# Optimization experiments

Measured on AMD Instinct MI355X. Metric: run time of the kernel, lower is better.

## Reference

```python
import jax, jax.numpy as jnp
import numpy as np

EPS = 1e-5
C = 256
K = 3
K2 = K * K


def conv2d(x, w, b=None, groups=1):
    out = jax.lax.conv_general_dilated(
        x, w, (1, 1), 'VALID',
        dimension_numbers=('NCHW', 'OIHW', 'NCHW'),
        feature_group_count=groups)
    if b is not None:
        out = out + b[None, :, None, None]
    return out


def _bilinear_one(img, py, px):
    # img: [C,H,W]; py,px: [K2,ho,wo] float sampling coords (zero outside)
    _, H, W = img.shape
    y0 = jnp.floor(py)
    x0 = jnp.floor(px)
    dy = py - y0
    dx = px - x0
    y0i = y0.astype(jnp.int32)
    x0i = x0.astype(jnp.int32)

    def gather(yi, xi):
        valid = ((yi >= 0) & (yi < H) & (xi >= 0) & (xi < W)).astype(img.dtype)
        yc = jnp.clip(yi, 0, H - 1)
        xc = jnp.clip(xi, 0, W - 1)
        return img[:, yc, xc] * valid[None]  # [C,K2,ho,wo]

    w00 = (1 - dy) * (1 - dx)
    w01 = (1 - dy) * dx
    w10 = dy * (1 - dx)
    w11 = dy * dx
    return (gather(y0i, x0i) * w00[None] + gather(y0i, x0i + 1) * w01[None]
            + gather(y0i + 1, x0i) * w10[None] + gather(y0i + 1, x0i + 1) * w11[None])


def deform_conv(x, off_w, off_b, w, b):
    # ModulatedDeformConvPack: 3x3, stride=1, pad=0, dil=1, deformable_groups=1
    B, Cin, H, W = x.shape
    ho, wo = H - 2, W - 2
    om = conv2d(x, off_w, off_b)  # [B, 3*K2, ho, wo]
    o1, o2, m = om[:, :K2], om[:, K2:2 * K2], om[:, 2 * K2:]
    offset = jnp.concatenate([o1, o2], axis=1)  # [B, 2*K2, ho, wo]
    off_y = offset[:, 0::2]  # kernel reads y at channel 2k
    off_x = offset[:, 1::2]  # and x at channel 2k+1
    mask = jax.nn.sigmoid(m)  # [B,K2,ho,wo]
    ky, kx = jnp.meshgrid(jnp.arange(K), jnp.arange(K), indexing='ij')
    base_y = (ky.reshape(K2, 1, 1) + jnp.arange(ho).reshape(1, ho, 1)).astype(x.dtype)
    base_x = (kx.reshape(K2, 1, 1) + jnp.arange(wo).reshape(1, 1, wo)).astype(x.dtype)
    py = base_y[None] + off_y
    px = base_x[None] + off_x
    samples = jax.vmap(_bilinear_one)(x, py, px)  # [B,C,K2,ho,wo]
    samples = samples * mask[:, None]
    out = jnp.einsum('bckhw,ock->bohw', samples, w.reshape(w.shape[0], Cin, K2))
    return out + b[None, :, None, None]


def bn(x, g, b_, m, v):
    scale = g / jnp.sqrt(v + EPS)
    return (x - m[None, :, None, None]) * scale[None, :, None, None] + b_[None, :, None, None]


def xcorr(inst, exam):
    # batch-as-groups depthwise cross-correlation
    B = exam.shape[0]
    w = exam.reshape(B * C, 1, 18, 18)
    x = inst.reshape(1, B * C, 30, 30)
    out = jax.lax.conv_general_dilated(
        x, w, (1, 1), 'VALID',
        dimension_numbers=('NCHW', 'OIHW', 'NCHW'),
        feature_group_count=B * C)
    return out.reshape(B, C, 13, 13)


def _forward(examplar, instance, off_w, off_b, dcn_w, dcn_b,
             bn1_g, bn1_b, bn1_m, bn1_v,
             fus_w, fus_b, bn2_g, bn2_b, bn2_m, bn2_v,
             cls_w, cls_b, box_w, box_b):
    def head(x, i):  # deform conv + BN (eval)
        y = deform_conv(x, off_w[i], off_b[i], dcn_w[i], dcn_b[i])
        return bn(y, bn1_g[i], bn1_b[i], bn1_m[i], bn1_v[i])

    exam_cls = head(examplar, 0)
    inst_cls = head(instance, 1)
    exam_reg = head(examplar, 2)
    inst_reg = head(instance, 3)

    xc_cls = xcorr(inst_cls, exam_cls)
    xc_reg = xcorr(inst_reg, exam_reg)

    def fuse(x, i):  # 1x1 conv + BN + ReLU
        y = jnp.einsum('bchw,oc->bohw', x, fus_w[i]) + fus_b[i][None, :, None, None]
        return jax.nn.relu(bn(y, bn2_g[i], bn2_b[i], bn2_m[i], bn2_v[i]))

    f_cls = fuse(xc_cls, 0)
    f_reg = fuse(xc_reg, 1)

    cls_pred = jnp.einsum('bchw,oc->bohw', f_cls, cls_w) + cls_b[None, :, None, None]
    box_pred = jnp.einsum('bchw,oc->bohw', f_reg, box_w) + box_b[None, :, None, None]
    return cls_pred, box_pred


def setup_inputs() -> dict:
    key = jax.random.key(0)
    ks = jax.random.split(key, 24)
    B = 16
    d = {
        'examplar': jax.random.normal(ks[0], (B, C, 20, 20), jnp.float32),
        'instance': jax.random.normal(ks[1], (B, C, 32, 32), jnp.float32),
        # 4 deform heads: 0=exam_cls, 1=inst_cls, 2=exam_reg, 3=inst_reg
        'off_w': jax.random.normal(ks[2], (4, 3 * K2, C, K, K), jnp.float32) * 0.01,
        'off_b': jax.random.normal(ks[3], (4, 3 * K2), jnp.float32) * 0.01,
        'dcn_w': jax.random.normal(ks[4], (4, C, C, K, K), jnp.float32) * 0.05,
        'dcn_b': jax.random.normal(ks[5], (4, C), jnp.float32) * 0.05,
        'bn1_g': jax.random.uniform(ks[6], (4, C), jnp.float32) + 0.5,
        'bn1_b': jax.random.normal(ks[7], (4, C), jnp.float32) * 0.1,
        'bn1_m': jax.random.normal(ks[8], (4, C), jnp.float32) * 0.1,
        'bn1_v': jax.random.uniform(ks[9], (4, C), jnp.float32) + 0.5,
        # 2 fusion modules: 0=cls, 1=reg
        'fus_w': jax.random.normal(ks[10], (2, C, C), jnp.float32) * 0.05,
        'fus_b': jax.random.normal(ks[11], (2, C), jnp.float32) * 0.05,
        'bn2_g': jax.random.uniform(ks[12], (2, C), jnp.float32) + 0.5,
        'bn2_b': jax.random.normal(ks[13], (2, C), jnp.float32) * 0.1,
        'bn2_m': jax.random.normal(ks[14], (2, C), jnp.float32) * 0.1,
        'bn2_v': jax.random.uniform(ks[15], (2, C), jnp.float32) + 0.5,
        'cls_w': jax.random.normal(ks[16], (4, C), jnp.float32) * 0.05,
        'cls_b': jax.random.normal(ks[17], (4,), jnp.float32) * 0.05,
        'box_w': jax.random.normal(ks[18], (16, C), jnp.float32) * 0.05,
        'box_b': jax.random.normal(ks[19], (16,), jnp.float32) * 0.05,
    }
    return d


def reference(examplar, instance, off_w, off_b, dcn_w, dcn_b,
              bn1_g, bn1_b, bn1_m, bn1_v,
              fus_w, fus_b, bn2_g, bn2_b, bn2_m, bn2_v,
              cls_w, cls_b, box_w, box_b):
    return _forward(examplar, instance, off_w, off_b, dcn_w, dcn_b,
                    bn1_g, bn1_b, bn1_m, bn1_v,
                    fus_w, fus_b, bn2_g, bn2_b, bn2_m, bn2_v,
                    cls_w, cls_b, box_w, box_b)
```

## Files before the change

kernel.cpp:

```cpp
#include <hip/hip_runtime.h>
#include <math.h>

#define EPSBN 1e-5f

typedef _Float16 f16x8 __attribute__((ext_vector_type(8)));
typedef _Float16 f16x2 __attribute__((ext_vector_type(2)));
typedef float    f32x4 __attribute__((ext_vector_type(4)));

__device__ __forceinline__ f16x8 splat8(float v) {
  _Float16 h = (_Float16)v;
  return (f16x8){h, h, h, h, h, h, h, h};
}

__device__ __forceinline__ void tile_decode(int idx, int& h, int& tl) {
  if (idx < 6)       { h = 0; tl = idx; }
  else if (idx < 21) { h = 1; tl = idx - 6; }
  else if (idx < 27) { h = 2; tl = idx - 21; }
  else               { h = 3; tl = idx - 27; }
}

static constexpr size_t XF_EX = 0;
static constexpr size_t XF_IN = 819200;
static constexpr size_t WPK   = 2916352;
static constexpr size_t OWPK  = 4096000;
static constexpr size_t FWT   = 4243456;
static constexpr size_t OM0   = 4374528;
static constexpr size_t OM1   = 4514496;
static constexpr size_t OM2   = 4903296;
static constexpr size_t OM3   = 5043264;
static constexpr size_t HOUT0 = 5432064;
static constexpr size_t HOUT1 = 6759168;
static constexpr size_t HOUT2 = 10445568;
static constexpr size_t HOUT3 = 11772672;
static constexpr size_t XCB   = 15459072;

__global__ __launch_bounds__(256) void k_transpose(const float* __restrict__ in,
                                                   _Float16* __restrict__ out,
                                                   int H, int W) {
  int y = blockIdx.x, b = blockIdx.y;
  __shared__ float tile[32][257];
  int t = threadIdx.x;
  int x = t & 31, cb = t >> 5;
  for (int c0 = 0; c0 < 256; c0 += 8) {
    int c = c0 + cb;
    if (x < W) tile[x][c] = in[(((size_t)b * 256 + c) * H + y) * W + x];
  }
  __syncthreads();
  for (int x2 = 0; x2 < W; ++x2)
    out[((((size_t)b * H + y) * W + x2) << 8) + t] = (_Float16)tile[x2][t];
}

__global__ __launch_bounds__(256) void k_wpack(const float* __restrict__ w,
                                               _Float16* __restrict__ wp) {
  int idx = blockIdx.x * 256 + threadIdx.x;
  if (idx >= 4 * 9 * 8 * 16 * 64 * 8) return;
  int e  = idx & 7;
  int l  = (idx >> 3) & 63;
  int ot = (idx >> 9) & 15;
  int cs = (idx >> 13) & 7;
  int ht = idx >> 16;
  int tap = ht % 9, h = ht / 9;
  int o = ot * 16 + (l & 15);
  int c = cs * 32 + 8 * (l >> 4) + e;
  wp[idx] = (_Float16)w[((size_t)((h * 256 + o) * 256 + c)) * 9 + tap];
}

__global__ __launch_bounds__(256) void k_owpack(const float* __restrict__ w,
                                                _Float16* __restrict__ wp) {
  int idx = blockIdx.x * 256 + threadIdx.x;
  if (idx >= 4 * 9 * 8 * 2 * 64 * 8) return;
  int e  = idx & 7;
  int l  = (idx >> 3) & 63;
  int ot = (idx >> 9) & 1;
  int cs = (idx >> 10) & 7;
  int ht = idx >> 13;
  int tap = ht % 9, h = ht / 9;
  int o = ot * 16 + (l & 15);
  int c = cs * 32 + 8 * (l >> 4) + e;
  wp[idx] = (o < 27) ? (_Float16)w[((size_t)((h * 27 + o) * 256 + c)) * 9 + tap]
                     : (_Float16)0.f;
}

__global__ __launch_bounds__(256) void k_fwt(const float* __restrict__ w,
                                             float* __restrict__ wt) {
  int idx = blockIdx.x * 256 + threadIdx.x;
  int o = idx & 255, c = (idx >> 8) & 255, i = idx >> 16;
  wt[idx] = w[(i << 16) + (o << 8) + c];
}

__global__ __launch_bounds__(512) void k_offmfma(const _Float16* __restrict__ xh_ex,
                                                 const _Float16* __restrict__ xh_in,
                                                 const _Float16* __restrict__ owpk,
                                                 const float* __restrict__ off_b,
                                                 float* __restrict__ ws) {
  int h, tl;
  tile_decode(blockIdx.x, h, tl);
  const int b = blockIdx.y;
  const int HH[4] = {20, 32, 20, 32};
  const size_t OMO[4] = {OM0, OM1, OM2, OM3};
  const int H = HH[h], W = H, ho = H - 2, wo = W - 2, P = ho * wo;
  const int p0 = tl << 6;
  const _Float16* xh = ((h & 1) ? xh_in : xh_ex) + (((size_t)b * H * W) << 8);

  __shared__ __align__(16) _Float16 S[64 * 256];
  __shared__ int rowoff[64];

  const int t = threadIdx.x, lane = t & 63, wave = t >> 6;
  if (t < 64) {
    int p = min(p0 + t, P - 1);
    int i = p / wo, j = p - i * wo;
    rowoff[t] = (i * W + j) << 8;
  }
  const int ot = wave & 1, nn = wave >> 1;
  f32x4 acc = {0.f, 0.f, 0.f, 0.f};
  __syncthreads();

  const int o8 = t & 31;
  const int plb = t >> 5;
  for (int tap = 0; tap < 9; ++tap) {
    const int ky = tap / 3, kx = tap - ky * 3;
    const int koff = (ky * W + kx) << 8;
    #pragma unroll
    for (int it = 0; it < 4; ++it) {
      int pl = it * 16 + plb;
      f16x8 v = *(const f16x8*)(xh + rowoff[pl] + koff + o8 * 8);
      *(f16x8*)((char*)S + pl * 512 + ((o8 * 16) ^ ((pl & 7) << 4))) = v;
    }
    __syncthreads();
    #pragma unroll
    for (int cs = 0; cs < 8; ++cs) {
      int ksg = tap * 8 + cs;
      const _Float16* ab = owpk + ((size_t)((h * 72 + ksg) * 2 + ot)) * 512 + lane * 8;
      f16x8 a = *(const f16x8*)(ab);
      int prow = nn * 16 + (lane & 15);
      f16x8 bf = *(const f16x8*)((char*)S + prow * 512 +
                                 ((cs * 64 + ((lane >> 4) << 4)) ^ ((prow & 7) << 4)));
      acc = __builtin_amdgcn_mfma_f32_16x16x32_f16(a, bf, acc, 0, 0, 0);
    }
    __syncthreads();
  }
  float* om = ws + OMO[h] + (size_t)b * 27 * P;
  int p = p0 + nn * 16 + (lane & 15);
  if (p < P) {
    #pragma unroll
    for (int r = 0; r < 4; ++r) {
      int o = ot * 16 + 4 * (lane >> 4) + r;
      if (o < 27) om[o * P + p] = acc[r] + off_b[h * 27 + o];
    }
  }
}

__global__ __launch_bounds__(512) void k_dgemm(const _Float16* __restrict__ xh_ex,
                                               const _Float16* __restrict__ xh_in,
                                               const _Float16* __restrict__ wpk,
                                               float* __restrict__ ws,
                                               const float* __restrict__ dcn_b,
                                               const float* __restrict__ g1,
                                               const float* __restrict__ b1,
                                               const float* __restrict__ m1,
                                               const float* __restrict__ v1) {
  int h, tl;
  tile_decode(blockIdx.x, h, tl);
  const int HH4[4] = {20, 32, 20, 32};
  const size_t OMO[4] = {OM0, OM1, OM2, OM3};
  const size_t HOO[4] = {HOUT0, HOUT1, HOUT2, HOUT3};
  const int H = HH4[h], W = H, ho = H - 2, wo = W - 2, P = ho * wo;
  const int b = blockIdx.y;
  const int p0 = tl << 6;
  const _Float16* xh = (h & 1) ? xh_in : xh_ex;
  const float* om = ws + OMO[h] + (size_t)b * 27 * P;
  float* outp = ws + HOO[h] + (size_t)b * 256 * P;

  __shared__ float4 swt4[576];
  __shared__ int4   sad4[576];
  __shared__ __align__(16) _Float16 S[64 * 256];

  const int t = threadIdx.x, lane = t & 63, wave = t >> 6;

  for (int e = t; e < 576; e += 512) {
    int pl = e / 9, k = e - pl * 9;
    float w4[4] = {0.f, 0.f, 0.f, 0.f};
    int a4[4] = {0, 0, 0, 0};
    int p = p0 + pl;
    if (p < P) {
      int i = p / wo, j = p - i * wo;
      float oy = om[(2 * k) * P + p];
      float ox = om[(2 * k + 1) * P + p];
      float mm = om[(18 + k) * P + p];
      float msk = 1.f / (1.f + __expf(-mm));
      int ky = k / 3, kx = k - ky * 3;
      float py = (float)(ky + i) + oy;
      float px = (float)(kx + j) + ox;
      float fy = floorf(py), fx = floorf(px);
      int y0 = (int)fy, x0 = (int)fx;
      float dy = py - fy, dx = px - fx;
      #pragma unroll
      for (int q = 0; q < 4; ++q) {
        int yy = y0 + (q >> 1), xx = x0 + (q & 1);
        bool vld = (yy >= 0) && (yy < H) && (xx >= 0) && (xx < W);
        int yc = min(max(yy, 0), H - 1), xc = min(max(xx, 0), W - 1);
        float wq = ((q >> 1) ? dy : 1.f - dy) * ((q & 1) ? dx : 1.f - dx);
        w4[q] = vld ? wq * msk : 0.f;
        a4[q] = ((b * H + yc) * W + xc) << 8;
      }
    }
    swt4[e] = make_float4(w4[0], w4[1], w4[2], w4[3]);
    sad4[e] = make_int4(a4[0], a4[1], a4[2], a4[3]);
  }

  f32x4 acc[2][4];
  #pragma unroll
  for (int a = 0; a < 2; ++a)
    #pragma unroll
    for (int n = 0; n < 4; ++n) acc[a][n] = (f32x4){0.f, 0.f, 0.f, 0.f};

  __syncthreads();

  const int o8 = t & 31;
  const int plb = t >> 5;
  for (int tap = 0; tap < 9; ++tap) {
    #pragma unroll
    for (int it = 0; it < 4; ++it) {
      int pl = it * 16 + plb;
      float4 w4 = swt4[pl * 9 + tap];
      int4   a4 = sad4[pl * 9 + tap];
      const _Float16* xb = xh + o8 * 8;
      f16x8 x0 = *(const f16x8*)(xb + a4.x);
      f16x8 x1 = *(const f16x8*)(xb + a4.y);
      f16x8 x2 = *(const f16x8*)(xb + a4.z);
      f16x8 x3 = *(const f16x8*)(xb + a4.w);
      f16x8 s = x0 * splat8(w4.x) + x1 * splat8(w4.y) + x2 * splat8(w4.z) + x3 * splat8(w4.w);
      *(f16x8*)((char*)S + pl * 512 + ((o8 * 16) ^ ((pl & 7) << 4))) = s;
    }
    __syncthreads();
    #pragma unroll
    for (int cs = 0; cs < 8; ++cs) {
      int ksg = tap * 8 + cs;
      const _Float16* ab = wpk + ((size_t)(h * 72 + ksg) * 16 + wave * 2) * 512 + lane * 8;
      f16x8 A0 = *(const f16x8*)(ab);
      f16x8 A1 = *(const f16x8*)(ab + 512);
      f16x8 B[4];
      #pragma unroll
      for (int n = 0; n < 4; ++n) {
        int prow = n * 16 + (lane & 15);
        B[n] = *(const f16x8*)((char*)S + prow * 512 +
                               ((cs * 64 + ((lane >> 4) << 4)) ^ ((prow & 7) << 4)));
      }
      #pragma unroll
      for (int n = 0; n < 4; ++n) {
        acc[0][n] = __builtin_amdgcn_mfma_f32_16x16x32_f16(A0, B[n], acc[0][n], 0, 0, 0);
        acc[1][n] = __builtin_amdgcn_mfma_f32_16x16x32_f16(A1, B[n], acc[1][n], 0, 0, 0);
      }
    }
    __syncthreads();
  }

  #pragma unroll
  for (int a = 0; a < 2; ++a) {
    int obase = (wave * 2 + a) * 16 + 4 * (lane >> 4);
    #pragma unroll
    for (int r = 0; r < 4; ++r) {
      int o = obase + r;
      float al = g1[h * 256 + o] * rsqrtf(v1[h * 256 + o] + EPSBN);
      float be = (dcn_b[h * 256 + o] - m1[h * 256 + o]) * al + b1[h * 256 + o];
      #pragma unroll
      for (int n = 0; n < 4; ++n) {
        int p = p0 + n * 16 + (lane & 15);
        if (p < P) outp[(size_t)o * P + p] = fmaf(acc[a][n][r], al, be);
      }
    }
  }
}

__global__ __launch_bounds__(256) void k_xcorr3(float* __restrict__ ws) {
  const int br = blockIdx.y;
  const int bc0 = blockIdx.x << 4;
  const float* exg = ws + (br ? HOUT2 : HOUT0) + (size_t)bc0 * 324;
  const float* ing = ws + (br ? HOUT3 : HOUT1) + (size_t)bc0 * 900;
  __shared__ __align__(16) _Float16 exl[16 * 324];
  __shared__ __align__(16) _Float16 inl[16 * 960];
  const int t = threadIdx.x;
  for (int idx = t; idx < 16 * 324; idx += 256)
    exl[idx] = (_Float16)exg[idx];
  for (int idx = t; idx < 16 * 960; idx += 256) {
    int c = idx & 31;
    int rr = idx >> 5;
    inl[idx] = (c < 30) ? (_Float16)ing[rr * 30 + c] : (_Float16)0.f;
  }
  __syncthreads();
  const int lane = t & 63, wave = t >> 6;
  const int sub = lane / 13;
  const int i = lane - sub * 13;
  const bool active = sub < 4;
  const int bcl = wave * 4 + (active ? sub : 0);
  float acc[13];
  #pragma unroll
  for (int j = 0; j < 13; ++j) acc[j] = 0.f;
  const _Float16* inb = inl + bcl * 960;
  const _Float16* exb = exl + bcl * 324;
  for (int u = 0; u < 18; ++u) {
    float a[30];
    const _Float16* rp = inb + (i + u) * 32;
    #pragma unroll
    for (int x = 0; x < 15; ++x) {
      f16x2 pr = *(const f16x2*)(rp + 2 * x);
      a[2 * x] = (float)pr[0]; a[2 * x + 1] = (float)pr[1];
    }
    float e[18];
    const _Float16* ep = exb + u * 18;
    #pragma unroll
    for (int x = 0; x < 9; ++x) {
      f16x2 pr = *(const f16x2*)(ep + 2 * x);
      e[2 * x] = (float)pr[0]; e[2 * x + 1] = (float)pr[1];
    }
    #pragma unroll
    for (int v = 0; v < 18; ++v)
      #pragma unroll
      for (int j = 0; j < 13; ++j)
        acc[j] = fmaf(a[v + j], e[v], acc[j]);
  }
  if (active) {
    float* o = ws + XCB + ((size_t)(br * 4096 + bc0 + bcl)) * 169 + i * 13;
    #pragma unroll
    for (int j = 0; j < 13; ++j) o[j] = acc[j];
  }
}

__global__ __launch_bounds__(256) void k_fuse2(float* __restrict__ ws,
                                               const float* __restrict__ fus_b,
                                               const float* __restrict__ g2,
                                               const float* __restrict__ b2,
                                               const float* __restrict__ m2,
                                               const float* __restrict__ v2,
                                               const float* __restrict__ cls_w,
                                               const float* __restrict__ cls_b,
                                               const float* __restrict__ box_w,
                                               const float* __restrict__ box_b,
                                               float* __restrict__ out) {
  const int ij0 = blockIdx.x * 13;
  const int b = blockIdx.y;
  const int br = blockIdx.z;
  const int n_out = br ? 16 : 4;
  const float* ow = br ? box_w : cls_w;
  const float* ob = br ? box_b : cls_b;
  float* outp = out + (br ? (size_t)10816 : 0);

  __shared__ float xv[256 * 13];
  __shared__ float fv[13 * 257];
  const int t = threadIdx.x;
  const float* src = ws + XCB + ((size_t)br * 4096 + b * 256) * 169;
  for (int idx = t; idx < 256 * 13; idx += 256) {
    int c = idx / 13, j = idx - c * 13;
    xv[idx] = src[(size_t)c * 169 + ij0 + j];
  }
  __syncthreads();

  const float* fwt = ws + FWT + ((size_t)br << 16) + t;
  float acc[13];
  #pragma unroll
  for (int j = 0; j < 13; ++j) acc[j] = 0.f;
  for (int c = 0; c < 256; ++c) {
    float wv = fwt[c << 8];
    #pragma unroll
    for (int j = 0; j < 13; ++j)
      acc[j] = fmaf(wv, xv[c * 13 + j], acc[j]);
  }
  float s2 = g2[br * 256 + t] * rsqrtf(v2[br * 256 + t] + EPSBN);
  float fb = fus_b[br * 256 + t], mm = m2[br * 256 + t], bb = b2[br * 256 + t];
  #pragma unroll
  for (int j = 0; j < 13; ++j)
    fv[j * 257 + t] = fmaxf((acc[j] + fb - mm) * s2 + bb, 0.f);
  __syncthreads();

  const int g = t >> 4, l16 = t & 15;
  for (int wi = g; wi < 13 * n_out; wi += 16) {
    int j = wi / n_out, po = wi - j * n_out;
    float part = 0.f;
    #pragma unroll
    for (int q = 0; q < 16; ++q)
      part = fmaf(ow[(po << 8) + l16 + (q << 4)], fv[j * 257 + l16 + (q << 4)], part);
    #pragma unroll
    for (int off = 8; off; off >>= 1) part += __shfl_xor(part, off);
    if (l16 == 0)
      outp[((size_t)b * n_out + po) * 169 + ij0 + j] = part + ob[po];
  }
}

extern "C" void kernel_launch(void* const* d_in, const int* in_sizes, int n_in,
                              void* d_out, int out_size, void* d_ws, size_t ws_size,
                              hipStream_t stream) {
  const float* ex    = (const float*)d_in[0];
  const float* inst  = (const float*)d_in[1];
  const float* off_w = (const float*)d_in[2];
  const float* off_b = (const float*)d_in[3];
  const float* dcn_w = (const float*)d_in[4];
  const float* dcn_b = (const float*)d_in[5];
  const float* bn1_g = (const float*)d_in[6];
  const float* bn1_b = (const float*)d_in[7];
  const float* bn1_m = (const float*)d_in[8];
  const float* bn1_v = (const float*)d_in[9];
  const float* fus_w = (const float*)d_in[10];
  const float* fus_b = (const float*)d_in[11];
  const float* bn2_g = (const float*)d_in[12];
  const float* bn2_b = (const float*)d_in[13];
  const float* bn2_m = (const float*)d_in[14];
  const float* bn2_v = (const float*)d_in[15];
  const float* cls_w = (const float*)d_in[16];
  const float* cls_b = (const float*)d_in[17];
  const float* box_w = (const float*)d_in[18];
  const float* box_b = (const float*)d_in[19];
  float* out = (float*)d_out;
  float* ws  = (float*)d_ws;

  _Float16* xh_ex = (_Float16*)(ws + XF_EX);
  _Float16* xh_in = (_Float16*)(ws + XF_IN);
  _Float16* wpk   = (_Float16*)(ws + WPK);
  _Float16* owpk  = (_Float16*)(ws + OWPK);

  k_transpose<<<dim3(20, 16), 256, 0, stream>>>(ex,   xh_ex, 20, 20);
  k_transpose<<<dim3(32, 16), 256, 0, stream>>>(inst, xh_in, 32, 32);
  k_wpack <<<9216, 256, 0, stream>>>(dcn_w, wpk);
  k_owpack<<<1152, 256, 0, stream>>>(off_w, owpk);
  k_fwt   <<<512, 256, 0, stream>>>(fus_w, ws + FWT);
  k_offmfma<<<dim3(42, 16), 512, 0, stream>>>(xh_ex, xh_in, owpk, off_b, ws);
  k_dgemm<<<dim3(42, 16), 512, 0, stream>>>(xh_ex, xh_in, wpk, ws,
                                            dcn_b, bn1_g, bn1_b, bn1_m, bn1_v);
  k_xcorr3<<<dim3(256, 2), 256, 0, stream>>>(ws);
  k_fuse2<<<dim3(13, 16, 2), 256, 0, stream>>>(ws, fus_b, bn2_g, bn2_b, bn2_m, bn2_v,
                                               cls_w, cls_b, box_w, box_b, out);
}
```

Baseline: 330.1 us.

## Fuse offset conv into deformable GEMM kernel and prefetch next-tap gathers

Merges the offset/mask convolution kernel into the deformable GEMM kernel, so offsets for each 64-pixel tile stay in shared memory instead of going through a global workspace. It also software-pipelines both tap loops by loading the next tap's inputs into registers while the MFMAs for the current tap run. Launch bounds now request 4 blocks per CU, and the grid becomes 1D with batch folded in. The costs are more registers (16 f16x8 prefetch buffers), more shared memory per block, and the offset conv being recomputed per tile exactly as before, with one fewer launch.

```diff
diff --git a/kernel.cpp b/kernel.cpp
--- a/kernel.cpp
+++ b/kernel.cpp
@@ -10,13 +10,6 @@
 __device__ __forceinline__ f16x8 splat8(float v) {
   _Float16 h = (_Float16)v;
   return (f16x8){h, h, h, h, h, h, h, h};
-}
-
-__device__ __forceinline__ void tile_decode(int idx, int& h, int& tl) {
-  if (idx < 6)       { h = 0; tl = idx; }
-  else if (idx < 21) { h = 1; tl = idx - 6; }
-  else if (idx < 27) { h = 2; tl = idx - 21; }
-  else               { h = 3; tl = idx - 27; }
 }
 
 static constexpr size_t XF_EX = 0;
@@ -24,10 +17,6 @@
 static constexpr size_t WPK   = 2916352;
 static constexpr size_t OWPK  = 4096000;
 static constexpr size_t FWT   = 4243456;
-static constexpr size_t OM0   = 4374528;
-static constexpr size_t OM1   = 4514496;
-static constexpr size_t OM2   = 4903296;
-static constexpr size_t OM3   = 5043264;
 static constexpr size_t HOUT0 = 5432064;
 static constexpr size_t HOUT1 = 6759168;
 static constexpr size_t HOUT2 = 10445568;
@@ -88,94 +77,91 @@
   wt[idx] = w[(i << 16) + (o << 8) + c];
 }
 
-__global__ __launch_bounds__(512) void k_offmfma(const _Float16* __restrict__ xh_ex,
+__global__ __launch_bounds__(512, 4) void k_head(const _Float16* __restrict__ xh_ex,
                                                  const _Float16* __restrict__ xh_in,
                                                  const _Float16* __restrict__ owpk,
+                                                 const _Float16* __restrict__ wpk,
                                                  const float* __restrict__ off_b,
-                                                 float* __restrict__ ws) {
-  int h, tl;
-  tile_decode(blockIdx.x, h, tl);
-  const int b = blockIdx.y;
-  const int HH[4] = {20, 32, 20, 32};
-  const size_t OMO[4] = {OM0, OM1, OM2, OM3};
-  const int H = HH[h], W = H, ho = H - 2, wo = W - 2, P = ho * wo;
+                                                 float* __restrict__ ws,
+                                                 const float* __restrict__ dcn_b,
+                                                 const float* __restrict__ g1,
+                                                 const float* __restrict__ b1,
+                                                 const float* __restrict__ m1,
+                                                 const float* __restrict__ v1) {
+  int idx = blockIdx.x;
+  int h, b, tl;
+  if (idx < 96)       { h = 0; b = idx / 6;              tl = idx - 6 * b; }
+  else if (idx < 336) { h = 1; int r = idx - 96;  b = r / 15; tl = r - 15 * b; }
+  else if (idx < 432) { h = 2; int r = idx - 336; b = r / 6;  tl = r - 6 * b; }
+  else                { h = 3; int r = idx - 432; b = r / 15; tl = r - 15 * b; }
+  const int HH4[4] = {20, 32, 20, 32};
+  const size_t HOO[4] = {HOUT0, HOUT1, HOUT2, HOUT3};
+  const int H = HH4[h], W = H, ho = H - 2, wo = W - 2, P = ho * wo;
   const int p0 = tl << 6;
-  const _Float16* xh = ((h & 1) ? xh_in : xh_ex) + (((size_t)b * H * W) << 8);
+  const _Float16* xh  = (h & 1) ? xh_in : xh_ex;
+  const _Float16* xhb = xh + (((size_t)b * H * W) << 8);
+  float* outp = ws + HOO[h] + (size_t)b * 256 * P;
 
   __shared__ __align__(16) _Float16 S[64 * 256];
-  __shared__ int rowoff[64];
+  __shared__ float4 swt4[576];
+  __shared__ int4   sad4[576];
+  __shared__ float  om_l[27][65];
+  __shared__ int    rowoff[64];
 
   const int t = threadIdx.x, lane = t & 63, wave = t >> 6;
+  const int o8 = t & 31, plb = t >> 5;
+  const int ot = wave & 1, nn = wave >> 1;
+
   if (t < 64) {
     int p = min(p0 + t, P - 1);
     int i = p / wo, j = p - i * wo;
     rowoff[t] = (i * W + j) << 8;
   }
-  const int ot = wave & 1, nn = wave >> 1;
-  f32x4 acc = {0.f, 0.f, 0.f, 0.f};
-  __syncthreads();
-
-  const int o8 = t & 31;
-  const int plb = t >> 5;
+  __syncthreads();
+
+  f32x4 accO = {0.f, 0.f, 0.f, 0.f};
+  f16x8 gr[4];
+  #pragma unroll
+  for (int it = 0; it < 4; ++it) {
+    int pl = it * 16 + plb;
+    gr[it] = *(const f16x8*)(xhb + rowoff[pl] + o8 * 8);
+  }
   for (int tap = 0; tap < 9; ++tap) {
-    const int ky = tap / 3, kx = tap - ky * 3;
-    const int koff = (ky * W + kx) << 8;
     #pragma unroll
     for (int it = 0; it < 4; ++it) {
       int pl = it * 16 + plb;
-      f16x8 v = *(const f16x8*)(xh + rowoff[pl] + koff + o8 * 8);
-      *(f16x8*)((char*)S + pl * 512 + ((o8 * 16) ^ ((pl & 7) << 4))) = v;
+      *(f16x8*)((char*)S + pl * 512 + ((o8 * 16) ^ ((pl & 7) << 4))) = gr[it];
     }
     __syncthreads();
+    if (tap < 8) {
+      int ky = (tap + 1) / 3, kx = (tap + 1) - ky * 3;
+      int koff = (ky * W + kx) << 8;
+      #pragma unroll
+      for (int it = 0; it < 4; ++it) {
+        int pl = it * 16 + plb;
+        gr[it] = *(const f16x8*)(xhb + rowoff[pl] + koff + o8 * 8);
+      }
+    }
     #pragma unroll
     for (int cs = 0; cs < 8; ++cs) {
       int ksg = tap * 8 + cs;
-      const _Float16* ab = owpk + ((size_t)((h * 72 + ksg) * 2 + ot)) * 512 + lane * 8;
-      f16x8 a = *(const f16x8*)(ab);
+      f16x8 a = *(const f16x8*)(owpk + ((size_t)((h * 72 + ksg) * 2 + ot)) * 512 + lane * 8);
       int prow = nn * 16 + (lane & 15);
       f16x8 bf = *(const f16x8*)((char*)S + prow * 512 +
                                  ((cs * 64 + ((lane >> 4) << 4)) ^ ((prow & 7) << 4)));
-      acc = __builtin_amdgcn_mfma_f32_16x16x32_f16(a, bf, acc, 0, 0, 0);
+      accO = __builtin_amdgcn_mfma_f32_16x16x32_f16(a, bf, accO, 0, 0, 0);
     }
     __syncthreads();
   }
-  float* om = ws + OMO[h] + (size_t)b * 27 * P;
-  int p = p0 + nn * 16 + (lane & 15);
-  if (p < P) {
+  {
+    int pcol = nn * 16 + (lane & 15);
     #pragma unroll
     for (int r = 0; r < 4; ++r) {
       int o = ot * 16 + 4 * (lane >> 4) + r;
-      if (o < 27) om[o * P + p] = acc[r] + off_b[h * 27 + o];
-    }
-  }
-}
-
-__global__ __launch_bounds__(512) void k_dgemm(const _Float16* __restrict__ xh_ex,
-                                               const _Float16* __restrict__ xh_in,
-                                               const _Float16* __restrict__ wpk,
-                                               float* __restrict__ ws,
-                                               const float* __restrict__ dcn_b,
-                                               const float* __restrict__ g1,
-                                               const float* __restrict__ b1,
-                                               const float* __restrict__ m1,
-                                               const float* __restrict__ v1) {
-  int h, tl;
-  tile_decode(blockIdx.x, h, tl);
-  const int HH4[4] = {20, 32, 20, 32};
-  const size_t OMO[4] = {OM0, OM1, OM2, OM3};
-  const size_t HOO[4] = {HOUT0, HOUT1, HOUT2, HOUT3};
-  const int H = HH4[h], W = H, ho = H - 2, wo = W - 2, P = ho * wo;
-  const int b = blockIdx.y;
-  const int p0 = tl << 6;
-  const _Float16* xh = (h & 1) ? xh_in : xh_ex;
-  const float* om = ws + OMO[h] + (size_t)b * 27 * P;
-  float* outp = ws + HOO[h] + (size_t)b * 256 * P;
-
-  __shared__ float4 swt4[576];
-  __shared__ int4   sad4[576];
-  __shared__ __align__(16) _Float16 S[64 * 256];
-
-  const int t = threadIdx.x, lane = t & 63, wave = t >> 6;
+      if (o < 27) om_l[o][pcol] = accO[r] + off_b[h * 27 + o];
+    }
+  }
+  __syncthreads();
 
   for (int e = t; e < 576; e += 512) {
     int pl = e / 9, k = e - pl * 9;
@@ -184,9 +170,9 @@
     int p = p0 + pl;
     if (p < P) {
       int i = p / wo, j = p - i * wo;
-      float oy = om[(2 * k) * P + p];
-      float ox = om[(2 * k + 1) * P + p];
-      float mm = om[(18 + k) * P + p];
+      float oy = om_l[2 * k][pl];
+      float ox = om_l[2 * k + 1][pl];
+      float mm = om_l[18 + k][pl];
       float msk = 1.f / (1.f + __expf(-mm));
       int ky = k / 3, kx = k - ky * 3;
       float py = (float)(ky + i) + oy;
@@ -213,26 +199,42 @@
   for (int a = 0; a < 2; ++a)
     #pragma unroll
     for (int n = 0; n < 4; ++n) acc[a][n] = (f32x4){0.f, 0.f, 0.f, 0.f};
-
-  __syncthreads();
-
-  const int o8 = t & 31;
-  const int plb = t >> 5;
+  __syncthreads();
+
+  const _Float16* xb = xh + o8 * 8;
+  f16x8 gx[16];
+  #pragma unroll
+  for (int it = 0; it < 4; ++it) {
+    int e = (it * 16 + plb) * 9;
+    int4 a4 = sad4[e];
+    gx[it * 4 + 0] = *(const f16x8*)(xb + a4.x);
+    gx[it * 4 + 1] = *(const f16x8*)(xb + a4.y);
+    gx[it * 4 + 2] = *(const f16x8*)(xb + a4.z);
+    gx[it * 4 + 3] = *(const f16x8*)(xb + a4.w);
+  }
   for (int tap = 0; tap < 9; ++tap) {
     #pragma unroll
     for (int it = 0; it < 4; ++it) {
       int pl = it * 16 + plb;
       float4 w4 = swt4[pl * 9 + tap];
-      int4   a4 = sad4[pl * 9 + tap];
-      const _Float16* xb = xh + o8 * 8;
-      f16x8 x0 = *(const f16x8*)(xb + a4.x);
-      f16x8 x1 = *(const f16x8*)(xb + a4.y);
-      f16x8 x2 = *(const f16x8*)(xb + a4.z);
-      f16x8 x3 = *(const f16x8*)(xb + a4.w);
-      f16x8 s = x0 * splat8(w4.x) + x1 * splat8(w4.y) + x2 * splat8(w4.z) + x3 * splat8(w4.w);
+      f16x8 s = gx[it * 4 + 0] * splat8(w4.x);
+      s = gx[it * 4 + 1] * splat8(w4.y) + s;
+      s = gx[it * 4 + 2] * splat8(w4.z) + s;
+      s = gx[it * 4 + 3] * splat8(w4.w) + s;
       *(f16x8*)((char*)S + pl * 512 + ((o8 * 16) ^ ((pl & 7) << 4))) = s;
     }
     __syncthreads();
+    if (tap < 8) {
+      #pragma unroll
+      for (int it = 0; it < 4; ++it) {
+        int e = (it * 16 + plb) * 9 + tap + 1;
+        int4 a4 = sad4[e];
+        gx[it * 4 + 0] = *(const f16x8*)(xb + a4.x);
+        gx[it * 4 + 1] = *(const f16x8*)(xb + a4.y);
+        gx[it * 4 + 2] = *(const f16x8*)(xb + a4.z);
+        gx[it * 4 + 3] = *(const f16x8*)(xb + a4.w);
+      }
+    }
     #pragma unroll
     for (int cs = 0; cs < 8; ++cs) {
       int ksg = tap * 8 + cs;
@@ -422,9 +424,8 @@
   k_wpack <<<9216, 256, 0, stream>>>(dcn_w, wpk);
   k_owpack<<<1152, 256, 0, stream>>>(off_w, owpk);
   k_fwt   <<<512, 256, 0, stream>>>(fus_w, ws + FWT);
-  k_offmfma<<<dim3(42, 16), 512, 0, stream>>>(xh_ex, xh_in, owpk, off_b, ws);
-  k_dgemm<<<dim3(42, 16), 512, 0, stream>>>(xh_ex, xh_in, wpk, ws,
-                                            dcn_b, bn1_g, bn1_b, bn1_m, bn1_v);
+  k_head<<<672, 512, 0, stream>>>(xh_ex, xh_in, owpk, wpk, off_b, ws,
+                                  dcn_b, bn1_g, bn1_b, bn1_m, bn1_v);
   k_xcorr3<<<dim3(256, 2), 256, 0, stream>>>(ws);
   k_fuse2<<<dim3(13, 16, 2), 256, 0, stream>>>(ws, fus_b, bn2_g, bn2_b, bn2_m, bn2_v,
                                                cls_w, cls_b, box_w, box_b, out);
```

Result: slower. 386.4 us (+17.0%).

## Load offset-conv operands directly from global and halve dgemm block size

Applied to the files above, without the earlier changes.

The offset conv kernel no longer stages input through shared memory with barriers. Each wave now loads its B fragments directly from the channel-last fp16 input and computes both output tiles with two MFMAs per step. The deformable GEMM kernel drops to 256 threads, with each wave covering four output tiles instead of two, which doubles the sampling work per thread. The grid becomes a 3D launch with early exit for unused tiles. This trades LDS traffic and barriers for more global loads, higher register pressure and fewer waves per block.

```diff
diff --git a/kernel.cpp b/kernel.cpp
--- a/kernel.cpp
+++ b/kernel.cpp
@@ -10,13 +10,6 @@
 __device__ __forceinline__ f16x8 splat8(float v) {
   _Float16 h = (_Float16)v;
   return (f16x8){h, h, h, h, h, h, h, h};
-}
-
-__device__ __forceinline__ void tile_decode(int idx, int& h, int& tl) {
-  if (idx < 6)       { h = 0; tl = idx; }
-  else if (idx < 21) { h = 1; tl = idx - 6; }
-  else if (idx < 27) { h = 2; tl = idx - 21; }
-  else               { h = 3; tl = idx - 27; }
 }
 
 static constexpr size_t XF_EX = 0;
@@ -88,69 +81,53 @@
   wt[idx] = w[(i << 16) + (o << 8) + c];
 }
 
-__global__ __launch_bounds__(512) void k_offmfma(const _Float16* __restrict__ xh_ex,
-                                                 const _Float16* __restrict__ xh_in,
-                                                 const _Float16* __restrict__ owpk,
-                                                 const float* __restrict__ off_b,
-                                                 float* __restrict__ ws) {
-  int h, tl;
-  tile_decode(blockIdx.x, h, tl);
-  const int b = blockIdx.y;
+__global__ __launch_bounds__(256) void k_offdirect(const _Float16* __restrict__ xh_ex,
+                                                   const _Float16* __restrict__ xh_in,
+                                                   const _Float16* __restrict__ owpk,
+                                                   const float* __restrict__ off_b,
+                                                   float* __restrict__ ws) {
+  const int h = blockIdx.z, b = blockIdx.y;
   const int HH[4] = {20, 32, 20, 32};
   const size_t OMO[4] = {OM0, OM1, OM2, OM3};
   const int H = HH[h], W = H, ho = H - 2, wo = W - 2, P = ho * wo;
-  const int p0 = tl << 6;
+  const int nblk = (P + 63) >> 6;
+  if (blockIdx.x >= nblk) return;
+  const int p0 = blockIdx.x << 6;
   const _Float16* xh = ((h & 1) ? xh_in : xh_ex) + (((size_t)b * H * W) << 8);
 
-  __shared__ __align__(16) _Float16 S[64 * 256];
-  __shared__ int rowoff[64];
-
   const int t = threadIdx.x, lane = t & 63, wave = t >> 6;
-  if (t < 64) {
-    int p = min(p0 + t, P - 1);
-    int i = p / wo, j = p - i * wo;
-    rowoff[t] = (i * W + j) << 8;
-  }
-  const int ot = wave & 1, nn = wave >> 1;
-  f32x4 acc = {0.f, 0.f, 0.f, 0.f};
-  __syncthreads();
-
-  const int o8 = t & 31;
-  const int plb = t >> 5;
+  int p = min(p0 + wave * 16 + (lane & 15), P - 1);
+  int i = p / wo, j = p - i * wo;
+  const _Float16* xrow = xh + ((i * W + j) << 8) + 8 * (lane >> 4);
+
+  f32x4 acc0 = {0.f, 0.f, 0.f, 0.f}, acc1 = {0.f, 0.f, 0.f, 0.f};
   for (int tap = 0; tap < 9; ++tap) {
-    const int ky = tap / 3, kx = tap - ky * 3;
-    const int koff = (ky * W + kx) << 8;
-    #pragma unroll
-    for (int it = 0; it < 4; ++it) {
-      int pl = it * 16 + plb;
-      f16x8 v = *(const f16x8*)(xh + rowoff[pl] + koff + o8 * 8);
-      *(f16x8*)((char*)S + pl * 512 + ((o8 * 16) ^ ((pl & 7) << 4))) = v;
-    }
-    __syncthreads();
+    int ky = tap / 3, kx = tap - ky * 3;
+    const _Float16* xt = xrow + ((ky * W + kx) << 8);
+    const _Float16* ab0 = owpk + ((size_t)(h * 72 + tap * 8) * 2) * 512 + lane * 8;
     #pragma unroll
     for (int cs = 0; cs < 8; ++cs) {
-      int ksg = tap * 8 + cs;
-      const _Float16* ab = owpk + ((size_t)((h * 72 + ksg) * 2 + ot)) * 512 + lane * 8;
-      f16x8 a = *(const f16x8*)(ab);
-      int prow = nn * 16 + (lane & 15);
-      f16x8 bf = *(const f16x8*)((char*)S + prow * 512 +
-                                 ((cs * 64 + ((lane >> 4) << 4)) ^ ((prow & 7) << 4)));
-      acc = __builtin_amdgcn_mfma_f32_16x16x32_f16(a, bf, acc, 0, 0, 0);
-    }
-    __syncthreads();
+      f16x8 bf = *(const f16x8*)(xt + cs * 32);
+      f16x8 a0 = *(const f16x8*)(ab0 + (size_t)cs * 1024);
+      f16x8 a1 = *(const f16x8*)(ab0 + (size_t)cs * 1024 + 512);
+      acc0 = __builtin_amdgcn_mfma_f32_16x16x32_f16(a0, bf, acc0, 0, 0, 0);
+      acc1 = __builtin_amdgcn_mfma_f32_16x16x32_f16(a1, bf, acc1, 0, 0, 0);
+    }
   }
   float* om = ws + OMO[h] + (size_t)b * 27 * P;
-  int p = p0 + nn * 16 + (lane & 15);
+  p = p0 + wave * 16 + (lane & 15);
   if (p < P) {
     #pragma unroll
     for (int r = 0; r < 4; ++r) {
-      int o = ot * 16 + 4 * (lane >> 4) + r;
-      if (o < 27) om[o * P + p] = acc[r] + off_b[h * 27 + o];
-    }
-  }
-}
-
-__global__ __launch_bounds__(512) void k_dgemm(const _Float16* __restrict__ xh_ex,
+      int o = 4 * (lane >> 4) + r;
+      if (o < 27) om[o * P + p] = acc0[r] + off_b[h * 27 + o];
+      int o2 = o + 16;
+      if (o2 < 27) om[o2 * P + p] = acc1[r] + off_b[h * 27 + o2];
+    }
+  }
+}
+
+__global__ __launch_bounds__(256) void k_dgemm(const _Float16* __restrict__ xh_ex,
                                                const _Float16* __restrict__ xh_in,
                                                const _Float16* __restrict__ wpk,
                                                float* __restrict__ ws,
@@ -159,14 +136,15 @@
                                                const float* __restrict__ b1,
                                                const float* __restrict__ m1,
                                                const float* __restrict__ v1) {
-  int h, tl;
-  tile_decode(blockIdx.x, h, tl);
+  const int h = blockIdx.z;
   const int HH4[4] = {20, 32, 20, 32};
   const size_t OMO[4] = {OM0, OM1, OM2, OM3};
   const size_t HOO[4] = {HOUT0, HOUT1, HOUT2, HOUT3};
   const int H = HH4[h], W = H, ho = H - 2, wo = W - 2, P = ho * wo;
+  const int nblk = (P + 63) >> 6;
+  if (blockIdx.x >= nblk) return;
   const int b = blockIdx.y;
-  const int p0 = tl << 6;
+  const int p0 = blockIdx.x << 6;
   const _Float16* xh = (h & 1) ? xh_in : xh_ex;
   const float* om = ws + OMO[h] + (size_t)b * 27 * P;
   float* outp = ws + HOO[h] + (size_t)b * 256 * P;
@@ -177,7 +155,7 @@
 
   const int t = threadIdx.x, lane = t & 63, wave = t >> 6;
 
-  for (int e = t; e < 576; e += 512) {
+  for (int e = t; e < 576; e += 256) {
     int pl = e / 9, k = e - pl * 9;
     float w4[4] = {0.f, 0.f, 0.f, 0.f};
     int a4[4] = {0, 0, 0, 0};
@@ -197,31 +175,30 @@
       #pragma unroll
       for (int q = 0; q < 4; ++q) {
         int yy = y0 + (q >> 1), xx = x0 + (q & 1);
-        bool vld = (yy >= 0) && (yy < H) && (xx >= 0) && (xx < W);
+        bool vld = (yy >= 0) && (yy < H) && (xx < W) && (xx >= 0);
         int yc = min(max(yy, 0), H - 1), xc = min(max(xx, 0), W - 1);
         float wq = ((q >> 1) ? dy : 1.f - dy) * ((q & 1) ? dx : 1.f - dx);
         w4[q] = vld ? wq * msk : 0.f;
-        a4[q] = ((b * H + yc) * W + xc) << 8;
+        a4[q] = ((blockIdx.y * H + yc) * W + xc) << 8;
       }
     }
     swt4[e] = make_float4(w4[0], w4[1], w4[2], w4[3]);
     sad4[e] = make_int4(a4[0], a4[1], a4[2], a4[3]);
   }
 
-  f32x4 acc[2][4];
+  f32x4 acc[4][4];
   #pragma unroll
-  for (int a = 0; a < 2; ++a)
+  for (int a = 0; a < 4; ++a)
     #pragma unroll
     for (int n = 0; n < 4; ++n) acc[a][n] = (f32x4){0.f, 0.f, 0.f, 0.f};
 
   __syncthreads();
 
   const int o8 = t & 31;
-  const int plb = t >> 5;
   for (int tap = 0; tap < 9; ++tap) {
     #pragma unroll
-    for (int it = 0; it < 4; ++it) {
-      int pl = it * 16 + plb;
+    for (int it = 0; it < 8; ++it) {
+      int pl = it * 8 + (t >> 5);
       float4 w4 = swt4[pl * 9 + tap];
       int4   a4 = sad4[pl * 9 + tap];
       const _Float16* xb = xh + o8 * 8;
@@ -236,9 +213,11 @@
     #pragma unroll
     for (int cs = 0; cs < 8; ++cs) {
       int ksg = tap * 8 + cs;
-      const _Float16* ab = wpk + ((size_t)(h * 72 + ksg) * 16 + wave * 2) * 512 + lane * 8;
+      const _Float16* ab = wpk + ((size_t)(h * 72 + ksg) * 16 + wave * 4) * 512 + lane * 8;
       f16x8 A0 = *(const f16x8*)(ab);
       f16x8 A1 = *(const f16x8*)(ab + 512);
+      f16x8 A2 = *(const f16x8*)(ab + 1024);
+      f16x8 A3 = *(const f16x8*)(ab + 1536);
       f16x8 B[4];
       #pragma unroll
       for (int n = 0; n < 4; ++n) {
@@ -250,14 +229,16 @@
       for (int n = 0; n < 4; ++n) {
         acc[0][n] = __builtin_amdgcn_mfma_f32_16x16x32_f16(A0, B[n], acc[0][n], 0, 0, 0);
         acc[1][n] = __builtin_amdgcn_mfma_f32_16x16x32_f16(A1, B[n], acc[1][n], 0, 0, 0);
+        acc[2][n] = __builtin_amdgcn_mfma_f32_16x16x32_f16(A2, B[n], acc[2][n], 0, 0, 0);
+        acc[3][n] = __builtin_amdgcn_mfma_f32_16x16x32_f16(A3, B[n], acc[3][n], 0, 0, 0);
       }
     }
     __syncthreads();
   }
 
   #pragma unroll
-  for (int a = 0; a < 2; ++a) {
-    int obase = (wave * 2 + a) * 16 + 4 * (lane >> 4);
+  for (int a = 0; a < 4; ++a) {
+    int obase = (wave * 4 + a) * 16 + 4 * (lane >> 4);
     #pragma unroll
     for (int r = 0; r < 4; ++r) {
       int o = obase + r;
@@ -422,9 +403,9 @@
   k_wpack <<<9216, 256, 0, stream>>>(dcn_w, wpk);
   k_owpack<<<1152, 256, 0, stream>>>(off_w, owpk);
   k_fwt   <<<512, 256, 0, stream>>>(fus_w, ws + FWT);
-  k_offmfma<<<dim3(42, 16), 512, 0, stream>>>(xh_ex, xh_in, owpk, off_b, ws);
-  k_dgemm<<<dim3(42, 16), 512, 0, stream>>>(xh_ex, xh_in, wpk, ws,
-                                            dcn_b, bn1_g, bn1_b, bn1_m, bn1_v);
+  k_offdirect<<<dim3(15, 16, 4), 256, 0, stream>>>(xh_ex, xh_in, owpk, off_b, ws);
+  k_dgemm<<<dim3(15, 16, 4), 256, 0, stream>>>(xh_ex, xh_in, wpk, ws,
+                                               dcn_b, bn1_g, bn1_b, bn1_m, bn1_v);
   k_xcorr3<<<dim3(256, 2), 256, 0, stream>>>(ws);
   k_fuse2<<<dim3(13, 16, 2), 256, 0, stream>>>(ws, fus_b, bn2_g, bn2_b, bn2_m, bn2_v,
                                                cls_w, cls_b, box_w, box_b, out);
```

Measured after the change: 341.4 us. +3.4%, slower.
